# Optimization experiments

Measured on AMD Instinct MI355X. Metric: run time of the kernel, lower is better.

Reference implementation:

```python
import jax, jax.numpy as jnp
import numpy as np

B, S, DM = 8, 1024, 512   # batch, seq_len, model dim
H, D = 8, 64              # n_heads, per-head dim


def setup_inputs() -> dict:
    key = jax.random.key(0)
    k1, k2, k3, k4, k5 = jax.random.split(key, 5)
    sc = 1.0 / np.sqrt(DM)
    return {
        "x": jax.random.normal(k1, (B, S, DM), dtype=jnp.float32),
        "Wq": jax.random.normal(k2, (H, DM, D), dtype=jnp.float32) * sc,
        "Wk": jax.random.normal(k3, (H, DM, D), dtype=jnp.float32) * sc,
        "Wv": jax.random.normal(k4, (H, DM, D), dtype=jnp.float32) * sc,
        "Wo": jax.random.normal(k5, (H * D, DM), dtype=jnp.float32) * (1.0 / np.sqrt(H * D)),
    }


def reference(x, Wq, Wk, Wv, Wo):
    # Batched multi-head attention equivalent to the per-head Python loop.
    q = jnp.einsum("bsm,hmd->bhsd", x, Wq)
    k = jnp.einsum("bsm,hmd->bhsd", x, Wk)
    v = jnp.einsum("bsm,hmd->bhsd", x, Wv)
    scores = jnp.einsum("bhsd,bhtd->bhst", q, k) / jnp.sqrt(jnp.float32(D))
    attn = jax.nn.softmax(scores, axis=-1)          # [B,H,S,S]
    heads = jnp.einsum("bhst,bhtd->bhsd", attn, v)  # [B,H,S,D]
    # concat heads along feature dim (head order matches loop order)
    concat = heads.transpose(0, 2, 1, 3).reshape(B, S, H * D)
    z = jnp.einsum("bsf,fm->bsm", concat, Wo)       # output projection
    return z, attn
```

## Files before the change

### kernel.cpp

```cpp
#include <hip/hip_runtime.h>

#define B 8
#define S 1024
#define DM 512
#define H 8
#define D 64

typedef __attribute__((ext_vector_type(8))) short bf16x8;
typedef __attribute__((ext_vector_type(4))) float f32x4;

__device__ inline f32x4 mfma16(bf16x8 a, bf16x8 b, f32x4 c) {
  return __builtin_amdgcn_mfma_f32_16x16x32_bf16(a, b, c, 0, 0, 0);
}

__device__ inline ushort f2bf(float f) {
  uint u = __float_as_uint(f);
  u += 0x7fff + ((u >> 16) & 1);
  return (ushort)(u >> 16);
}

__global__ __launch_bounds__(256) void cast_x_kernel(const float* __restrict__ x,
                                                     ushort* __restrict__ xbf) {
  int idx = blockIdx.x * 256 + threadIdx.x;
  float4 v = *(const float4*)(x + (size_t)idx * 4);
  ushort4 o;
  o.x = f2bf(v.x); o.y = f2bf(v.y); o.z = f2bf(v.z); o.w = f2bf(v.w);
  *(ushort4*)(xbf + (size_t)idx * 4) = o;
}

__global__ __launch_bounds__(256) void prep_w_kernel(
    const float* __restrict__ Wq, const float* __restrict__ Wk,
    const float* __restrict__ Wv, const float* __restrict__ Wo,
    ushort* __restrict__ WT, ushort* __restrict__ WoT) {
  int idx = blockIdx.x * 256 + threadIdx.x;
  if (idx < 1536 * 512) {
    int f = idx >> 9, m = idx & 511;
    int g = f >> 9, fl = f & 511, h = fl >> 6, d = fl & 63;
    const float* W = (g == 0) ? Wq : (g == 1) ? Wk : Wv;
    WT[idx] = f2bf(W[((size_t)h * DM + m) * D + d]);
  } else {
    int i2 = idx - 1536 * 512;
    int m = i2 >> 9, f = i2 & 511;
    WoT[(size_t)m * 512 + f] = f2bf(Wo[(size_t)f * DM + m]);
  }
}

__global__ __launch_bounds__(256) void qkv_gemm_kernel(
    const ushort* __restrict__ A, const ushort* __restrict__ Bm,
    ushort* __restrict__ qb, ushort* __restrict__ kb, ushort* __restrict__ vt) {
  __shared__ ushort As[64][72], Bs[64][72];
  const int tid = threadIdx.x;
  const int m0 = blockIdx.x * 64, n0 = blockIdx.y * 64;
  const int w = tid >> 6, l = tid & 63;
  const int r = l & 15, q = l >> 4;
  const int mh = (w >> 1) * 32, nh = (w & 1) * 32;

  f32x4 acc[2][2] = {};
  const int srow = tid >> 2, sco = (tid & 3) * 16;

  for (int k0 = 0; k0 < 512; k0 += 64) {
    const ushort* ap = A + (size_t)(m0 + srow) * 512 + k0 + sco;
    const ushort* bp = Bm + (size_t)(n0 + srow) * 512 + k0 + sco;
    uint4 a0 = *(const uint4*)ap;
    uint4 a1 = *(const uint4*)(ap + 8);
    uint4 b0 = *(const uint4*)bp;
    uint4 b1 = *(const uint4*)(bp + 8);
    __syncthreads();
    *(uint4*)&As[srow][sco] = a0;
    *(uint4*)&As[srow][sco + 8] = a1;
    *(uint4*)&Bs[srow][sco] = b0;
    *(uint4*)&Bs[srow][sco + 8] = b1;
    __syncthreads();
    #pragma unroll
    for (int kk = 0; kk < 64; kk += 32) {
      bf16x8 fa0 = *(const bf16x8*)&As[mh + r][kk + q * 8];
      bf16x8 fa1 = *(const bf16x8*)&As[mh + 16 + r][kk + q * 8];
      bf16x8 fb0 = *(const bf16x8*)&Bs[nh + r][kk + q * 8];
      bf16x8 fb1 = *(const bf16x8*)&Bs[nh + 16 + r][kk + q * 8];
      acc[0][0] = mfma16(fa0, fb0, acc[0][0]);
      acc[0][1] = mfma16(fa0, fb1, acc[0][1]);
      acc[1][0] = mfma16(fa1, fb0, acc[1][0]);
      acc[1][1] = mfma16(fa1, fb1, acc[1][1]);
    }
  }

  const int g = n0 >> 9;
  #pragma unroll
  for (int mi = 0; mi < 2; ++mi)
    #pragma unroll
    for (int nj = 0; nj < 2; ++nj)
      #pragma unroll
      for (int i = 0; i < 4; ++i) {
        int row = m0 + mh + mi * 16 + q * 4 + i;
        int col = n0 + nh + nj * 16 + r;
        int bb = row >> 10, s = row & 1023;
        int fl = col & 511, h = fl >> 6, d = fl & 63;
        ushort val = f2bf(acc[mi][nj][i]);
        if (g == 0)
          qb[(((size_t)bb * H + h) * S + s) * D + d] = val;
        else if (g == 1)
          kb[(((size_t)bb * H + h) * S + s) * D + d] = val;
        else
          vt[(((size_t)bb * H + h) * D + d) * S + s] = val;
      }
}

__global__ __launch_bounds__(256, 4) void attn_kernel(
    const ushort* __restrict__ qb, const ushort* __restrict__ kb,
    const ushort* __restrict__ vt, float* __restrict__ attn,
    ushort* __restrict__ concat) {
  __shared__ ushort Pl[16 * 1024];
  __shared__ float redm[4][16], redsum[4][16];
  const int tid = threadIdx.x;
  const int w = tid >> 6, l = tid & 63;
  const int r = l & 15, q = l >> 4;
  const int s0 = blockIdx.x * 16, bh = blockIdx.y;

  const ushort* qp = qb + ((size_t)bh * S + s0) * D;
  bf16x8 qa0 = *(const bf16x8*)(qp + r * 64 + q * 8);
  bf16x8 qa1 = *(const bf16x8*)(qp + r * 64 + 32 + q * 8);

  const ushort* kp = kb + (size_t)bh * S * D;
  f32x4 sc[16];
  #pragma unroll
  for (int kt = 0; kt < 16; ++kt) {
    const ushort* kr = kp + (size_t)(w * 256 + kt * 16 + r) * 64 + q * 8;
    bf16x8 kf0 = *(const bf16x8*)kr;
    bf16x8 kf1 = *(const bf16x8*)(kr + 32);
    f32x4 a = {};
    a = mfma16(qa0, kf0, a);
    a = mfma16(qa1, kf1, a);
    sc[kt] = a * 0.125f;
  }

  float mx[4];
  #pragma unroll
  for (int i = 0; i < 4; ++i) {
    float m = sc[0][i];
    #pragma unroll
    for (int kt = 1; kt < 16; ++kt) m = fmaxf(m, sc[kt][i]);
    #pragma unroll
    for (int msk = 1; msk < 16; msk <<= 1) m = fmaxf(m, __shfl_xor(m, msk));
    mx[i] = m;
  }
  if (r == 0) {
    #pragma unroll
    for (int i = 0; i < 4; ++i) redm[w][q * 4 + i] = mx[i];
  }
  __syncthreads();
  #pragma unroll
  for (int i = 0; i < 4; ++i)
    mx[i] = fmaxf(fmaxf(redm[0][q * 4 + i], redm[1][q * 4 + i]),
                  fmaxf(redm[2][q * 4 + i], redm[3][q * 4 + i]));

  float sm[4] = {0.f, 0.f, 0.f, 0.f};
  #pragma unroll
  for (int kt = 0; kt < 16; ++kt)
    #pragma unroll
    for (int i = 0; i < 4; ++i) {
      float e = __expf(sc[kt][i] - mx[i]);
      sc[kt][i] = e;
      sm[i] += e;
    }
  #pragma unroll
  for (int i = 0; i < 4; ++i) {
    float s = sm[i];
    #pragma unroll
    for (int msk = 1; msk < 16; msk <<= 1) s += __shfl_xor(s, msk);
    sm[i] = s;
  }
  if (r == 0) {
    #pragma unroll
    for (int i = 0; i < 4; ++i) redsum[w][q * 4 + i] = sm[i];
  }
  __syncthreads();
  float rinv[4];
  #pragma unroll
  for (int i = 0; i < 4; ++i)
    rinv[i] = 1.0f / (redsum[0][q * 4 + i] + redsum[1][q * 4 + i] +
                      redsum[2][q * 4 + i] + redsum[3][q * 4 + i]);

  float* ap = attn + ((size_t)bh * S + s0) * S;
  #pragma unroll
  for (int kt = 0; kt < 16; ++kt) {
    int col = w * 256 + kt * 16 + r;
    #pragma unroll
    for (int i = 0; i < 4; ++i) {
      int row = q * 4 + i;
      ap[(size_t)row * S + col] = sc[kt][i] * rinv[i];
      Pl[row * 1024 + (col ^ ((row & 7) << 3))] = f2bf(sc[kt][i]);
    }
  }
  __syncthreads();

  {
    const int d0 = w * 16;
    const ushort* vp = vt + ((size_t)bh * D + d0 + r) * S;
    f32x4 acc[4] = {};
    #pragma unroll
    for (int stp = 0; stp < 32; ++stp) {
      int t0 = stp * 32 + q * 8;
      bf16x8 pa = *(const bf16x8*)&Pl[r * 1024 + (t0 ^ ((r & 7) << 3))];
      bf16x8 vb = *(const bf16x8*)(vp + t0);
      acc[stp & 3] = mfma16(pa, vb, acc[stp & 3]);
    }
    f32x4 tot = acc[0] + acc[1] + acc[2] + acc[3];
    const int b = bh >> 3, h = bh & 7;
    #pragma unroll
    for (int i = 0; i < 4; ++i)
      concat[((size_t)b * S + s0 + q * 4 + i) * DM + h * D + d0 + r] =
          f2bf(tot[i] * rinv[i]);
  }
}

__global__ __launch_bounds__(256) void outproj_gemm_kernel(
    const ushort* __restrict__ A, const ushort* __restrict__ Bm,
    float* __restrict__ z) {
  __shared__ ushort As[64][72], Bs[64][72];
  const int tid = threadIdx.x;
  const int m0 = blockIdx.x * 64, n0 = blockIdx.y * 64;
  const int w = tid >> 6, l = tid & 63;
  const int r = l & 15, q = l >> 4;
  const int mh = (w >> 1) * 32, nh = (w & 1) * 32;

  f32x4 acc[2][2] = {};
  const int srow = tid >> 2, sco = (tid & 3) * 16;

  for (int k0 = 0; k0 < 512; k0 += 64) {
    const ushort* ap = A + (size_t)(m0 + srow) * 512 + k0 + sco;
    const ushort* bp = Bm + (size_t)(n0 + srow) * 512 + k0 + sco;
    uint4 a0 = *(const uint4*)ap;
    uint4 a1 = *(const uint4*)(ap + 8);
    uint4 b0 = *(const uint4*)bp;
    uint4 b1 = *(const uint4*)(bp + 8);
    __syncthreads();
    *(uint4*)&As[srow][sco] = a0;
    *(uint4*)&As[srow][sco + 8] = a1;
    *(uint4*)&Bs[srow][sco] = b0;
    *(uint4*)&Bs[srow][sco + 8] = b1;
    __syncthreads();
    #pragma unroll
    for (int kk = 0; kk < 64; kk += 32) {
      bf16x8 fa0 = *(const bf16x8*)&As[mh + r][kk + q * 8];
      bf16x8 fa1 = *(const bf16x8*)&As[mh + 16 + r][kk + q * 8];
      bf16x8 fb0 = *(const bf16x8*)&Bs[nh + r][kk + q * 8];
      bf16x8 fb1 = *(const bf16x8*)&Bs[nh + 16 + r][kk + q * 8];
      acc[0][0] = mfma16(fa0, fb0, acc[0][0]);
      acc[0][1] = mfma16(fa0, fb1, acc[0][1]);
      acc[1][0] = mfma16(fa1, fb0, acc[1][0]);
      acc[1][1] = mfma16(fa1, fb1, acc[1][1]);
    }
  }

  #pragma unroll
  for (int mi = 0; mi < 2; ++mi)
    #pragma unroll
    for (int nj = 0; nj < 2; ++nj)
      #pragma unroll
      for (int i = 0; i < 4; ++i) {
        int row = m0 + mh + mi * 16 + q * 4 + i;
        int col = n0 + nh + nj * 16 + r;
        z[(size_t)row * DM + col] = acc[mi][nj][i];
      }
}

extern "C" void kernel_launch(void* const* d_in, const int* in_sizes, int n_in,
                              void* d_out, int out_size, void* d_ws, size_t ws_size,
                              hipStream_t stream) {
  const float* x  = (const float*)d_in[0];
  const float* Wq = (const float*)d_in[1];
  const float* Wk = (const float*)d_in[2];
  const float* Wv = (const float*)d_in[3];
  const float* Wo = (const float*)d_in[4];

  float* z    = (float*)d_out;
  float* attn = z + (size_t)B * S * DM;

  ushort* xbf    = (ushort*)d_ws;
  ushort* WT     = xbf + (size_t)8192 * 512;
  ushort* WoT    = WT + (size_t)1536 * 512;
  ushort* qb     = WoT + (size_t)512 * 512;
  ushort* kb     = qb + (size_t)B * H * S * D;
  ushort* vt     = kb + (size_t)B * H * S * D;
  ushort* concat = vt + (size_t)B * H * S * D;

  cast_x_kernel<<<(B * S * DM / 4 + 255) / 256, 256, 0, stream>>>(x, xbf);
  prep_w_kernel<<<(1536 * 512 + 512 * 512) / 256, 256, 0, stream>>>(
      Wq, Wk, Wv, Wo, WT, WoT);
  qkv_gemm_kernel<<<dim3(8192 / 64, 1536 / 64), 256, 0, stream>>>(
      xbf, WT, qb, kb, vt);
  attn_kernel<<<dim3(S / 16, B * H), 256, 0, stream>>>(
      qb, kb, vt, attn, concat);
  outproj_gemm_kernel<<<dim3(8192 / 64, 512 / 64), 256, 0, stream>>>(
      concat, WoT, z);
}
```

Measured before the change: 190.3 us.

## Enlarge GEMM tiles to 128x128, use direct global-to-LDS loads, merge prep kernels

Both projection GEMMs move from 64x64 to 128x128 block tiles, with each wave computing a 4x4 grid of MFMA tiles for more operand reuse. Operands are staged through global_load_lds instead of register round-trips, and the LDS row padding is removed, which can cause bank conflicts. The x cast and weight transposes are merged into one prep kernel whose weight reads are now coalesced. The out-projection grid shrinks to 256 blocks, which may underfill the GPU's compute units.

```diff
diff --git a/kernel.cpp b/kernel.cpp
--- a/kernel.cpp
+++ b/kernel.cpp
@@ -19,28 +19,34 @@
   return (ushort)(u >> 16);
 }
 
-__global__ __launch_bounds__(256) void cast_x_kernel(const float* __restrict__ x,
-                                                     ushort* __restrict__ xbf) {
-  int idx = blockIdx.x * 256 + threadIdx.x;
-  float4 v = *(const float4*)(x + (size_t)idx * 4);
-  ushort4 o;
-  o.x = f2bf(v.x); o.y = f2bf(v.y); o.z = f2bf(v.z); o.w = f2bf(v.w);
-  *(ushort4*)(xbf + (size_t)idx * 4) = o;
-}
-
-__global__ __launch_bounds__(256) void prep_w_kernel(
-    const float* __restrict__ Wq, const float* __restrict__ Wk,
-    const float* __restrict__ Wv, const float* __restrict__ Wo,
+#define GLOAD16(gp, lp)                                                  \
+  __builtin_amdgcn_global_load_lds(                                      \
+      (const __attribute__((address_space(1))) void*)(gp),               \
+      (__attribute__((address_space(3))) void*)(lp), 16, 0, 0)
+
+__global__ __launch_bounds__(256) void prep_kernel(
+    const float* __restrict__ x, const float* __restrict__ Wq,
+    const float* __restrict__ Wk, const float* __restrict__ Wv,
+    const float* __restrict__ Wo, ushort* __restrict__ xbf,
     ushort* __restrict__ WT, ushort* __restrict__ WoT) {
-  int idx = blockIdx.x * 256 + threadIdx.x;
-  if (idx < 1536 * 512) {
-    int f = idx >> 9, m = idx & 511;
-    int g = f >> 9, fl = f & 511, h = fl >> 6, d = fl & 63;
+  const int bid = blockIdx.x;
+  if (bid < 4096) {
+    int idx = bid * 256 + threadIdx.x;
+    float4 v = *(const float4*)(x + (size_t)idx * 4);
+    ushort4 o;
+    o.x = f2bf(v.x); o.y = f2bf(v.y); o.z = f2bf(v.z); o.w = f2bf(v.w);
+    *(ushort4*)(xbf + (size_t)idx * 4) = o;
+  } else if (bid < 7168) {
+    int idx = (bid - 4096) * 256 + threadIdx.x;
+    int g = idx >> 18;
+    int rem = idx & 262143;
     const float* W = (g == 0) ? Wq : (g == 1) ? Wk : Wv;
-    WT[idx] = f2bf(W[((size_t)h * DM + m) * D + d]);
+    float val = W[rem];
+    int d = rem & 63, m = (rem >> 6) & 511, h = rem >> 15;
+    WT[((size_t)(g << 9) + (h << 6) + d) * 512 + m] = f2bf(val);
   } else {
-    int i2 = idx - 1536 * 512;
-    int m = i2 >> 9, f = i2 & 511;
+    int idx = (bid - 7168) * 256 + threadIdx.x;
+    int m = idx & 511, f = idx >> 9;
     WoT[(size_t)m * 512 + f] = f2bf(Wo[(size_t)f * DM + m]);
   }
 }
@@ -48,51 +54,52 @@
 __global__ __launch_bounds__(256) void qkv_gemm_kernel(
     const ushort* __restrict__ A, const ushort* __restrict__ Bm,
     ushort* __restrict__ qb, ushort* __restrict__ kb, ushort* __restrict__ vt) {
-  __shared__ ushort As[64][72], Bs[64][72];
+  __shared__ ushort As[128 * 64], Bs[128 * 64];
   const int tid = threadIdx.x;
-  const int m0 = blockIdx.x * 64, n0 = blockIdx.y * 64;
+  const int m0 = blockIdx.x * 128, n0 = blockIdx.y * 128;
   const int w = tid >> 6, l = tid & 63;
   const int r = l & 15, q = l >> 4;
-  const int mh = (w >> 1) * 32, nh = (w & 1) * 32;
-
-  f32x4 acc[2][2] = {};
-  const int srow = tid >> 2, sco = (tid & 3) * 16;
+  const int wr = (w >> 1) * 64, wc = (w & 1) * 64;
+
+  f32x4 acc[4][4] = {};
+  const int o0 = tid * 16;
 
   for (int k0 = 0; k0 < 512; k0 += 64) {
-    const ushort* ap = A + (size_t)(m0 + srow) * 512 + k0 + sco;
-    const ushort* bp = Bm + (size_t)(n0 + srow) * 512 + k0 + sco;
-    uint4 a0 = *(const uint4*)ap;
-    uint4 a1 = *(const uint4*)(ap + 8);
-    uint4 b0 = *(const uint4*)bp;
-    uint4 b1 = *(const uint4*)(bp + 8);
     __syncthreads();
-    *(uint4*)&As[srow][sco] = a0;
-    *(uint4*)&As[srow][sco + 8] = a1;
-    *(uint4*)&Bs[srow][sco] = b0;
-    *(uint4*)&Bs[srow][sco + 8] = b1;
+    #pragma unroll
+    for (int j = 0; j < 4; ++j) {
+      int o = j * 4096 + o0;
+      int row = o >> 7, cb = o & 127;
+      GLOAD16(A + (size_t)(m0 + row) * 512 + k0 + (cb >> 1), &As[o >> 1]);
+      GLOAD16(Bm + (size_t)(n0 + row) * 512 + k0 + (cb >> 1), &Bs[o >> 1]);
+    }
     __syncthreads();
     #pragma unroll
     for (int kk = 0; kk < 64; kk += 32) {
-      bf16x8 fa0 = *(const bf16x8*)&As[mh + r][kk + q * 8];
-      bf16x8 fa1 = *(const bf16x8*)&As[mh + 16 + r][kk + q * 8];
-      bf16x8 fb0 = *(const bf16x8*)&Bs[nh + r][kk + q * 8];
-      bf16x8 fb1 = *(const bf16x8*)&Bs[nh + 16 + r][kk + q * 8];
-      acc[0][0] = mfma16(fa0, fb0, acc[0][0]);
-      acc[0][1] = mfma16(fa0, fb1, acc[0][1]);
-      acc[1][0] = mfma16(fa1, fb0, acc[1][0]);
-      acc[1][1] = mfma16(fa1, fb1, acc[1][1]);
+      bf16x8 fa[4], fb[4];
+      #pragma unroll
+      for (int mi = 0; mi < 4; ++mi)
+        fa[mi] = *(const bf16x8*)&As[(wr + mi * 16 + r) * 64 + kk + q * 8];
+      #pragma unroll
+      for (int nj = 0; nj < 4; ++nj)
+        fb[nj] = *(const bf16x8*)&Bs[(wc + nj * 16 + r) * 64 + kk + q * 8];
+      #pragma unroll
+      for (int mi = 0; mi < 4; ++mi)
+        #pragma unroll
+        for (int nj = 0; nj < 4; ++nj)
+          acc[mi][nj] = mfma16(fa[mi], fb[nj], acc[mi][nj]);
     }
   }
 
   const int g = n0 >> 9;
   #pragma unroll
-  for (int mi = 0; mi < 2; ++mi)
-    #pragma unroll
-    for (int nj = 0; nj < 2; ++nj)
+  for (int mi = 0; mi < 4; ++mi)
+    #pragma unroll
+    for (int nj = 0; nj < 4; ++nj)
       #pragma unroll
       for (int i = 0; i < 4; ++i) {
-        int row = m0 + mh + mi * 16 + q * 4 + i;
-        int col = n0 + nh + nj * 16 + r;
+        int row = m0 + wr + mi * 16 + q * 4 + i;
+        int col = n0 + wc + nj * 16 + r;
         int bb = row >> 10, s = row & 1023;
         int fl = col & 511, h = fl >> 6, d = fl & 63;
         ushort val = f2bf(acc[mi][nj][i]);
@@ -216,50 +223,51 @@
 __global__ __launch_bounds__(256) void outproj_gemm_kernel(
     const ushort* __restrict__ A, const ushort* __restrict__ Bm,
     float* __restrict__ z) {
-  __shared__ ushort As[64][72], Bs[64][72];
+  __shared__ ushort As[128 * 64], Bs[128 * 64];
   const int tid = threadIdx.x;
-  const int m0 = blockIdx.x * 64, n0 = blockIdx.y * 64;
+  const int m0 = blockIdx.x * 128, n0 = blockIdx.y * 128;
   const int w = tid >> 6, l = tid & 63;
   const int r = l & 15, q = l >> 4;
-  const int mh = (w >> 1) * 32, nh = (w & 1) * 32;
-
-  f32x4 acc[2][2] = {};
-  const int srow = tid >> 2, sco = (tid & 3) * 16;
+  const int wr = (w >> 1) * 64, wc = (w & 1) * 64;
+
+  f32x4 acc[4][4] = {};
+  const int o0 = tid * 16;
 
   for (int k0 = 0; k0 < 512; k0 += 64) {
-    const ushort* ap = A + (size_t)(m0 + srow) * 512 + k0 + sco;
-    const ushort* bp = Bm + (size_t)(n0 + srow) * 512 + k0 + sco;
-    uint4 a0 = *(const uint4*)ap;
-    uint4 a1 = *(const uint4*)(ap + 8);
-    uint4 b0 = *(const uint4*)bp;
-    uint4 b1 = *(const uint4*)(bp + 8);
     __syncthreads();
-    *(uint4*)&As[srow][sco] = a0;
-    *(uint4*)&As[srow][sco + 8] = a1;
-    *(uint4*)&Bs[srow][sco] = b0;
-    *(uint4*)&Bs[srow][sco + 8] = b1;
+    #pragma unroll
+    for (int j = 0; j < 4; ++j) {
+      int o = j * 4096 + o0;
+      int row = o >> 7, cb = o & 127;
+      GLOAD16(A + (size_t)(m0 + row) * 512 + k0 + (cb >> 1), &As[o >> 1]);
+      GLOAD16(Bm + (size_t)(n0 + row) * 512 + k0 + (cb >> 1), &Bs[o >> 1]);
+    }
     __syncthreads();
     #pragma unroll
     for (int kk = 0; kk < 64; kk += 32) {
-      bf16x8 fa0 = *(const bf16x8*)&As[mh + r][kk + q * 8];
-      bf16x8 fa1 = *(const bf16x8*)&As[mh + 16 + r][kk + q * 8];
-      bf16x8 fb0 = *(const bf16x8*)&Bs[nh + r][kk + q * 8];
-      bf16x8 fb1 = *(const bf16x8*)&Bs[nh + 16 + r][kk + q * 8];
-      acc[0][0] = mfma16(fa0, fb0, acc[0][0]);
-      acc[0][1] = mfma16(fa0, fb1, acc[0][1]);
-      acc[1][0] = mfma16(fa1, fb0, acc[1][0]);
-      acc[1][1] = mfma16(fa1, fb1, acc[1][1]);
-    }
-  }
-
-  #pragma unroll
-  for (int mi = 0; mi < 2; ++mi)
-    #pragma unroll
-    for (int nj = 0; nj < 2; ++nj)
+      bf16x8 fa[4], fb[4];
+      #pragma unroll
+      for (int mi = 0; mi < 4; ++mi)
+        fa[mi] = *(const bf16x8*)&As[(wr + mi * 16 + r) * 64 + kk + q * 8];
+      #pragma unroll
+      for (int nj = 0; nj < 4; ++nj)
+        fb[nj] = *(const bf16x8*)&Bs[(wc + nj * 16 + r) * 64 + kk + q * 8];
+      #pragma unroll
+      for (int mi = 0; mi < 4; ++mi)
+        #pragma unroll
+        for (int nj = 0; nj < 4; ++nj)
+          acc[mi][nj] = mfma16(fa[mi], fb[nj], acc[mi][nj]);
+    }
+  }
+
+  #pragma unroll
+  for (int mi = 0; mi < 4; ++mi)
+    #pragma unroll
+    for (int nj = 0; nj < 4; ++nj)
       #pragma unroll
       for (int i = 0; i < 4; ++i) {
-        int row = m0 + mh + mi * 16 + q * 4 + i;
-        int col = n0 + nh + nj * 16 + r;
+        int row = m0 + wr + mi * 16 + q * 4 + i;
+        int col = n0 + wc + nj * 16 + r;
         z[(size_t)row * DM + col] = acc[mi][nj][i];
       }
 }
@@ -284,13 +292,11 @@
   ushort* vt     = kb + (size_t)B * H * S * D;
   ushort* concat = vt + (size_t)B * H * S * D;
 
-  cast_x_kernel<<<(B * S * DM / 4 + 255) / 256, 256, 0, stream>>>(x, xbf);
-  prep_w_kernel<<<(1536 * 512 + 512 * 512) / 256, 256, 0, stream>>>(
-      Wq, Wk, Wv, Wo, WT, WoT);
-  qkv_gemm_kernel<<<dim3(8192 / 64, 1536 / 64), 256, 0, stream>>>(
+  prep_kernel<<<8192, 256, 0, stream>>>(x, Wq, Wk, Wv, Wo, xbf, WT, WoT);
+  qkv_gemm_kernel<<<dim3(8192 / 128, 1536 / 128), 256, 0, stream>>>(
       xbf, WT, qb, kb, vt);
   attn_kernel<<<dim3(S / 16, B * H), 256, 0, stream>>>(
       qb, kb, vt, attn, concat);
-  outproj_gemm_kernel<<<dim3(8192 / 64, 512 / 64), 256, 0, stream>>>(
+  outproj_gemm_kernel<<<dim3(8192 / 128, 512 / 128), 256, 0, stream>>>(
       concat, WoT, z);
 }
```

Result: slower. 199.8 us (+5.0%).

## Fuse all stages into one persistent cooperative kernel with grid syncs

Applied to the files above, without the earlier changes.

Replaces the five separate launches (cast, weight prep, QKV GEMM, attention, output GEMM) with a single persistent cooperative kernel. Blocks loop over tiles for each stage and meet at grid-wide barriers between stages, with shared memory reused through a union. The weight-prep loop now reads the weights contiguously and scatters the transposed writes. This removes launch gaps and tail effects between stages, but adds grid-sync cost and caps concurrency at the occupancy-derived grid size (at most 1024 blocks).

```diff
diff --git a/kernel.cpp b/kernel.cpp
--- a/kernel.cpp
+++ b/kernel.cpp
@@ -1,4 +1,7 @@
 #include <hip/hip_runtime.h>
+#include <hip/hip_cooperative_groups.h>
+
+namespace cg = cooperative_groups;
 
 #define B 8
 #define S 1024
@@ -19,249 +22,258 @@
   return (ushort)(u >> 16);
 }
 
-__global__ __launch_bounds__(256) void cast_x_kernel(const float* __restrict__ x,
-                                                     ushort* __restrict__ xbf) {
-  int idx = blockIdx.x * 256 + threadIdx.x;
-  float4 v = *(const float4*)(x + (size_t)idx * 4);
-  ushort4 o;
-  o.x = f2bf(v.x); o.y = f2bf(v.y); o.z = f2bf(v.z); o.w = f2bf(v.w);
-  *(ushort4*)(xbf + (size_t)idx * 4) = o;
-}
-
-__global__ __launch_bounds__(256) void prep_w_kernel(
-    const float* __restrict__ Wq, const float* __restrict__ Wk,
-    const float* __restrict__ Wv, const float* __restrict__ Wo,
-    ushort* __restrict__ WT, ushort* __restrict__ WoT) {
-  int idx = blockIdx.x * 256 + threadIdx.x;
-  if (idx < 1536 * 512) {
-    int f = idx >> 9, m = idx & 511;
-    int g = f >> 9, fl = f & 511, h = fl >> 6, d = fl & 63;
-    const float* W = (g == 0) ? Wq : (g == 1) ? Wk : Wv;
-    WT[idx] = f2bf(W[((size_t)h * DM + m) * D + d]);
-  } else {
-    int i2 = idx - 1536 * 512;
-    int m = i2 >> 9, f = i2 & 511;
-    WoT[(size_t)m * 512 + f] = f2bf(Wo[(size_t)f * DM + m]);
-  }
-}
-
-__global__ __launch_bounds__(256) void qkv_gemm_kernel(
-    const ushort* __restrict__ A, const ushort* __restrict__ Bm,
-    ushort* __restrict__ qb, ushort* __restrict__ kb, ushort* __restrict__ vt) {
-  __shared__ ushort As[64][72], Bs[64][72];
+union SMem {
+  struct { ushort As[64][72]; ushort Bs[64][72]; } g;
+  struct { ushort Pl[16 * 1024];
+           float redm[4][16]; float redsum[4][16]; } a;
+};
+
+__global__ __launch_bounds__(256, 4) void mega_kernel(
+    const float* __restrict__ x, const float* __restrict__ Wq,
+    const float* __restrict__ Wk, const float* __restrict__ Wv,
+    const float* __restrict__ Wo, float* __restrict__ z,
+    float* __restrict__ attnO, ushort* __restrict__ xbf,
+    ushort* __restrict__ WT, ushort* __restrict__ WoT,
+    ushort* __restrict__ qb, ushort* __restrict__ kb,
+    ushort* __restrict__ vt, ushort* __restrict__ concat) {
+  __shared__ SMem sm;
+  cg::grid_group grid = cg::this_grid();
   const int tid = threadIdx.x;
-  const int m0 = blockIdx.x * 64, n0 = blockIdx.y * 64;
-  const int w = tid >> 6, l = tid & 63;
-  const int r = l & 15, q = l >> 4;
-  const int mh = (w >> 1) * 32, nh = (w & 1) * 32;
-
-  f32x4 acc[2][2] = {};
-  const int srow = tid >> 2, sco = (tid & 3) * 16;
-
-  for (int k0 = 0; k0 < 512; k0 += 64) {
-    const ushort* ap = A + (size_t)(m0 + srow) * 512 + k0 + sco;
-    const ushort* bp = Bm + (size_t)(n0 + srow) * 512 + k0 + sco;
-    uint4 a0 = *(const uint4*)ap;
-    uint4 a1 = *(const uint4*)(ap + 8);
-    uint4 b0 = *(const uint4*)bp;
-    uint4 b1 = *(const uint4*)(bp + 8);
-    __syncthreads();
-    *(uint4*)&As[srow][sco] = a0;
-    *(uint4*)&As[srow][sco + 8] = a1;
-    *(uint4*)&Bs[srow][sco] = b0;
-    *(uint4*)&Bs[srow][sco + 8] = b1;
-    __syncthreads();
-    #pragma unroll
-    for (int kk = 0; kk < 64; kk += 32) {
-      bf16x8 fa0 = *(const bf16x8*)&As[mh + r][kk + q * 8];
-      bf16x8 fa1 = *(const bf16x8*)&As[mh + 16 + r][kk + q * 8];
-      bf16x8 fb0 = *(const bf16x8*)&Bs[nh + r][kk + q * 8];
-      bf16x8 fb1 = *(const bf16x8*)&Bs[nh + 16 + r][kk + q * 8];
-      acc[0][0] = mfma16(fa0, fb0, acc[0][0]);
-      acc[0][1] = mfma16(fa0, fb1, acc[0][1]);
-      acc[1][0] = mfma16(fa1, fb0, acc[1][0]);
-      acc[1][1] = mfma16(fa1, fb1, acc[1][1]);
+  const int nthr = gridDim.x * 256;
+
+  {
+    const int NX = 1 << 20;
+    const int NWT = 3 * 8 * 512 * 64;
+    const int tot = NX + NWT + 512 * 512;
+    for (int idx = blockIdx.x * 256 + tid; idx < tot; idx += nthr) {
+      if (idx < NX) {
+        float4 v = *(const float4*)(x + (size_t)idx * 4);
+        ushort4 o;
+        o.x = f2bf(v.x); o.y = f2bf(v.y); o.z = f2bf(v.z); o.w = f2bf(v.w);
+        *(ushort4*)(xbf + (size_t)idx * 4) = o;
+      } else if (idx < NX + NWT) {
+        int i2 = idx - NX;
+        int g = i2 >> 18, rem = i2 & 262143;
+        const float* W = (g == 0) ? Wq : (g == 1) ? Wk : Wv;
+        float val = W[rem];
+        int d = rem & 63, m = (rem >> 6) & 511, h = rem >> 15;
+        WT[((size_t)(g << 9) + (h << 6) + d) * 512 + m] = f2bf(val);
+      } else {
+        int i2 = idx - NX - NWT;
+        int m = i2 & 511, f = i2 >> 9;
+        WoT[(size_t)m * 512 + f] = f2bf(Wo[(size_t)f * DM + m]);
+      }
     }
   }
-
-  const int g = n0 >> 9;
-  #pragma unroll
-  for (int mi = 0; mi < 2; ++mi)
-    #pragma unroll
-    for (int nj = 0; nj < 2; ++nj)
+  grid.sync();
+
+  {
+    const int w = tid >> 6, l = tid & 63;
+    const int r = l & 15, qq = l >> 4;
+    const int mh = (w >> 1) * 32, nh = (w & 1) * 32;
+    const int srow = tid >> 2, sco = (tid & 3) * 16;
+    for (int t = blockIdx.x; t < 3072; t += gridDim.x) {
+      const int m0 = (t & 127) * 64, n0 = (t >> 7) * 64;
+      f32x4 acc[2][2] = {};
+      for (int k0 = 0; k0 < 512; k0 += 64) {
+        const ushort* ap = xbf + (size_t)(m0 + srow) * 512 + k0 + sco;
+        const ushort* bp = WT + (size_t)(n0 + srow) * 512 + k0 + sco;
+        uint4 a0 = *(const uint4*)ap;
+        uint4 a1 = *(const uint4*)(ap + 8);
+        uint4 b0 = *(const uint4*)bp;
+        uint4 b1 = *(const uint4*)(bp + 8);
+        __syncthreads();
+        *(uint4*)&sm.g.As[srow][sco] = a0;
+        *(uint4*)&sm.g.As[srow][sco + 8] = a1;
+        *(uint4*)&sm.g.Bs[srow][sco] = b0;
+        *(uint4*)&sm.g.Bs[srow][sco + 8] = b1;
+        __syncthreads();
+        #pragma unroll
+        for (int kk = 0; kk < 64; kk += 32) {
+          bf16x8 fa0 = *(const bf16x8*)&sm.g.As[mh + r][kk + qq * 8];
+          bf16x8 fa1 = *(const bf16x8*)&sm.g.As[mh + 16 + r][kk + qq * 8];
+          bf16x8 fb0 = *(const bf16x8*)&sm.g.Bs[nh + r][kk + qq * 8];
+          bf16x8 fb1 = *(const bf16x8*)&sm.g.Bs[nh + 16 + r][kk + qq * 8];
+          acc[0][0] = mfma16(fa0, fb0, acc[0][0]);
+          acc[0][1] = mfma16(fa0, fb1, acc[0][1]);
+          acc[1][0] = mfma16(fa1, fb0, acc[1][0]);
+          acc[1][1] = mfma16(fa1, fb1, acc[1][1]);
+        }
+      }
+      const int g = n0 >> 9;
+      #pragma unroll
+      for (int mi = 0; mi < 2; ++mi)
+        #pragma unroll
+        for (int nj = 0; nj < 2; ++nj)
+          #pragma unroll
+          for (int i = 0; i < 4; ++i) {
+            int row = m0 + mh + mi * 16 + qq * 4 + i;
+            int col = n0 + nh + nj * 16 + r;
+            int bb = row >> 10, s = row & 1023;
+            int fl = col & 511, h = fl >> 6, d = fl & 63;
+            ushort val = f2bf(acc[mi][nj][i]);
+            if (g == 0)
+              qb[(((size_t)bb * H + h) * S + s) * D + d] = val;
+            else if (g == 1)
+              kb[(((size_t)bb * H + h) * S + s) * D + d] = val;
+            else
+              vt[(((size_t)bb * H + h) * D + d) * S + s] = val;
+          }
+    }
+  }
+  grid.sync();
+
+  {
+    const int w = tid >> 6, l = tid & 63;
+    const int r = l & 15, qq = l >> 4;
+    for (int t = blockIdx.x; t < 4096; t += gridDim.x) {
+      __syncthreads();
+      const int s0 = (t & 63) * 16, bh = t >> 6;
+
+      const ushort* qp = qb + ((size_t)bh * S + s0) * D;
+      bf16x8 qa0 = *(const bf16x8*)(qp + r * 64 + qq * 8);
+      bf16x8 qa1 = *(const bf16x8*)(qp + r * 64 + 32 + qq * 8);
+
+      const ushort* kp = kb + (size_t)bh * S * D;
+      f32x4 sc[16];
+      #pragma unroll
+      for (int kt = 0; kt < 16; ++kt) {
+        const ushort* kr = kp + (size_t)(w * 256 + kt * 16 + r) * 64 + qq * 8;
+        bf16x8 kf0 = *(const bf16x8*)kr;
+        bf16x8 kf1 = *(const bf16x8*)(kr + 32);
+        f32x4 a = {};
+        a = mfma16(qa0, kf0, a);
+        a = mfma16(qa1, kf1, a);
+        sc[kt] = a * 0.125f;
+      }
+
+      float mx[4];
       #pragma unroll
       for (int i = 0; i < 4; ++i) {
-        int row = m0 + mh + mi * 16 + q * 4 + i;
-        int col = n0 + nh + nj * 16 + r;
-        int bb = row >> 10, s = row & 1023;
-        int fl = col & 511, h = fl >> 6, d = fl & 63;
-        ushort val = f2bf(acc[mi][nj][i]);
-        if (g == 0)
-          qb[(((size_t)bb * H + h) * S + s) * D + d] = val;
-        else if (g == 1)
-          kb[(((size_t)bb * H + h) * S + s) * D + d] = val;
-        else
-          vt[(((size_t)bb * H + h) * D + d) * S + s] = val;
-      }
-}
-
-__global__ __launch_bounds__(256, 4) void attn_kernel(
-    const ushort* __restrict__ qb, const ushort* __restrict__ kb,
-    const ushort* __restrict__ vt, float* __restrict__ attn,
-    ushort* __restrict__ concat) {
-  __shared__ ushort Pl[16 * 1024];
-  __shared__ float redm[4][16], redsum[4][16];
-  const int tid = threadIdx.x;
-  const int w = tid >> 6, l = tid & 63;
-  const int r = l & 15, q = l >> 4;
-  const int s0 = blockIdx.x * 16, bh = blockIdx.y;
-
-  const ushort* qp = qb + ((size_t)bh * S + s0) * D;
-  bf16x8 qa0 = *(const bf16x8*)(qp + r * 64 + q * 8);
-  bf16x8 qa1 = *(const bf16x8*)(qp + r * 64 + 32 + q * 8);
-
-  const ushort* kp = kb + (size_t)bh * S * D;
-  f32x4 sc[16];
-  #pragma unroll
-  for (int kt = 0; kt < 16; ++kt) {
-    const ushort* kr = kp + (size_t)(w * 256 + kt * 16 + r) * 64 + q * 8;
-    bf16x8 kf0 = *(const bf16x8*)kr;
-    bf16x8 kf1 = *(const bf16x8*)(kr + 32);
-    f32x4 a = {};
-    a = mfma16(qa0, kf0, a);
-    a = mfma16(qa1, kf1, a);
-    sc[kt] = a * 0.125f;
-  }
-
-  float mx[4];
-  #pragma unroll
-  for (int i = 0; i < 4; ++i) {
-    float m = sc[0][i];
-    #pragma unroll
-    for (int kt = 1; kt < 16; ++kt) m = fmaxf(m, sc[kt][i]);
-    #pragma unroll
-    for (int msk = 1; msk < 16; msk <<= 1) m = fmaxf(m, __shfl_xor(m, msk));
-    mx[i] = m;
-  }
-  if (r == 0) {
-    #pragma unroll
-    for (int i = 0; i < 4; ++i) redm[w][q * 4 + i] = mx[i];
-  }
-  __syncthreads();
-  #pragma unroll
-  for (int i = 0; i < 4; ++i)
-    mx[i] = fmaxf(fmaxf(redm[0][q * 4 + i], redm[1][q * 4 + i]),
-                  fmaxf(redm[2][q * 4 + i], redm[3][q * 4 + i]));
-
-  float sm[4] = {0.f, 0.f, 0.f, 0.f};
-  #pragma unroll
-  for (int kt = 0; kt < 16; ++kt)
-    #pragma unroll
-    for (int i = 0; i < 4; ++i) {
-      float e = __expf(sc[kt][i] - mx[i]);
-      sc[kt][i] = e;
-      sm[i] += e;
+        float m = sc[0][i];
+        #pragma unroll
+        for (int kt = 1; kt < 16; ++kt) m = fmaxf(m, sc[kt][i]);
+        #pragma unroll
+        for (int msk = 1; msk < 16; msk <<= 1) m = fmaxf(m, __shfl_xor(m, msk));
+        mx[i] = m;
+      }
+      if (r == 0) {
+        #pragma unroll
+        for (int i = 0; i < 4; ++i) sm.a.redm[w][qq * 4 + i] = mx[i];
+      }
+      __syncthreads();
+      #pragma unroll
+      for (int i = 0; i < 4; ++i)
+        mx[i] = fmaxf(fmaxf(sm.a.redm[0][qq * 4 + i], sm.a.redm[1][qq * 4 + i]),
+                      fmaxf(sm.a.redm[2][qq * 4 + i], sm.a.redm[3][qq * 4 + i]));
+
+      float smv[4] = {0.f, 0.f, 0.f, 0.f};
+      #pragma unroll
+      for (int kt = 0; kt < 16; ++kt)
+        #pragma unroll
+        for (int i = 0; i < 4; ++i) {
+          float e = __expf(sc[kt][i] - mx[i]);
+          sc[kt][i] = e;
+          smv[i] += e;
+        }
+      #pragma unroll
+      for (int i = 0; i < 4; ++i) {
+        float s = smv[i];
+        #pragma unroll
+        for (int msk = 1; msk < 16; msk <<= 1) s += __shfl_xor(s, msk);
+        smv[i] = s;
+      }
+      if (r == 0) {
+        #pragma unroll
+        for (int i = 0; i < 4; ++i) sm.a.redsum[w][qq * 4 + i] = smv[i];
+      }
+      __syncthreads();
+      float rinv[4];
+      #pragma unroll
+      for (int i = 0; i < 4; ++i)
+        rinv[i] = 1.0f / (sm.a.redsum[0][qq * 4 + i] + sm.a.redsum[1][qq * 4 + i] +
+                          sm.a.redsum[2][qq * 4 + i] + sm.a.redsum[3][qq * 4 + i]);
+
+      float* ap = attnO + ((size_t)bh * S + s0) * S;
+      #pragma unroll
+      for (int kt = 0; kt < 16; ++kt) {
+        int col = w * 256 + kt * 16 + r;
+        #pragma unroll
+        for (int i = 0; i < 4; ++i) {
+          int row = qq * 4 + i;
+          ap[(size_t)row * S + col] = sc[kt][i] * rinv[i];
+          sm.a.Pl[row * 1024 + (col ^ ((row & 7) << 3))] = f2bf(sc[kt][i]);
+        }
+      }
+      __syncthreads();
+
+      {
+        const int d0 = w * 16;
+        const ushort* vp = vt + ((size_t)bh * D + d0 + r) * S;
+        f32x4 acc[4] = {};
+        #pragma unroll
+        for (int stp = 0; stp < 32; ++stp) {
+          int t0 = stp * 32 + qq * 8;
+          bf16x8 pa = *(const bf16x8*)&sm.a.Pl[r * 1024 + (t0 ^ ((r & 7) << 3))];
+          bf16x8 vb = *(const bf16x8*)(vp + t0);
+          acc[stp & 3] = mfma16(pa, vb, acc[stp & 3]);
+        }
+        f32x4 tot = acc[0] + acc[1] + acc[2] + acc[3];
+        const int b = t >> 9, h = (t >> 6) & 7;
+        #pragma unroll
+        for (int i = 0; i < 4; ++i)
+          concat[((size_t)b * S + s0 + qq * 4 + i) * DM + h * D + d0 + r] =
+              f2bf(tot[i] * rinv[i]);
+      }
     }
-  #pragma unroll
-  for (int i = 0; i < 4; ++i) {
-    float s = sm[i];
-    #pragma unroll
-    for (int msk = 1; msk < 16; msk <<= 1) s += __shfl_xor(s, msk);
-    sm[i] = s;
-  }
-  if (r == 0) {
-    #pragma unroll
-    for (int i = 0; i < 4; ++i) redsum[w][q * 4 + i] = sm[i];
-  }
-  __syncthreads();
-  float rinv[4];
-  #pragma unroll
-  for (int i = 0; i < 4; ++i)
-    rinv[i] = 1.0f / (redsum[0][q * 4 + i] + redsum[1][q * 4 + i] +
-                      redsum[2][q * 4 + i] + redsum[3][q * 4 + i]);
-
-  float* ap = attn + ((size_t)bh * S + s0) * S;
-  #pragma unroll
-  for (int kt = 0; kt < 16; ++kt) {
-    int col = w * 256 + kt * 16 + r;
-    #pragma unroll
-    for (int i = 0; i < 4; ++i) {
-      int row = q * 4 + i;
-      ap[(size_t)row * S + col] = sc[kt][i] * rinv[i];
-      Pl[row * 1024 + (col ^ ((row & 7) << 3))] = f2bf(sc[kt][i]);
+  }
+  grid.sync();
+
+  {
+    const int w = tid >> 6, l = tid & 63;
+    const int r = l & 15, qq = l >> 4;
+    const int mh = (w >> 1) * 32, nh = (w & 1) * 32;
+    const int srow = tid >> 2, sco = (tid & 3) * 16;
+    for (int t = blockIdx.x; t < 1024; t += gridDim.x) {
+      const int m0 = (t >> 3) * 64, n0 = (t & 7) * 64;
+      f32x4 acc[2][2] = {};
+      for (int k0 = 0; k0 < 512; k0 += 64) {
+        const ushort* ap = concat + (size_t)(m0 + srow) * 512 + k0 + sco;
+        const ushort* bp = WoT + (size_t)(n0 + srow) * 512 + k0 + sco;
+        uint4 a0 = *(const uint4*)ap;
+        uint4 a1 = *(const uint4*)(ap + 8);
+        uint4 b0 = *(const uint4*)bp;
+        uint4 b1 = *(const uint4*)(bp + 8);
+        __syncthreads();
+        *(uint4*)&sm.g.As[srow][sco] = a0;
+        *(uint4*)&sm.g.As[srow][sco + 8] = a1;
+        *(uint4*)&sm.g.Bs[srow][sco] = b0;
+        *(uint4*)&sm.g.Bs[srow][sco + 8] = b1;
+        __syncthreads();
+        #pragma unroll
+        for (int kk = 0; kk < 64; kk += 32) {
+          bf16x8 fa0 = *(const bf16x8*)&sm.g.As[mh + r][kk + qq * 8];
+          bf16x8 fa1 = *(const bf16x8*)&sm.g.As[mh + 16 + r][kk + qq * 8];
+          bf16x8 fb0 = *(const bf16x8*)&sm.g.Bs[nh + r][kk + qq * 8];
+          bf16x8 fb1 = *(const bf16x8*)&sm.g.Bs[nh + 16 + r][kk + qq * 8];
+          acc[0][0] = mfma16(fa0, fb0, acc[0][0]);
+          acc[0][1] = mfma16(fa0, fb1, acc[0][1]);
+          acc[1][0] = mfma16(fa1, fb0, acc[1][0]);
+          acc[1][1] = mfma16(fa1, fb1, acc[1][1]);
+        }
+      }
+      #pragma unroll
+      for (int mi = 0; mi < 2; ++mi)
+        #pragma unroll
+        for (int nj = 0; nj < 2; ++nj)
+          #pragma unroll
+          for (int i = 0; i < 4; ++i) {
+            int row = m0 + mh + mi * 16 + qq * 4 + i;
+            int col = n0 + nh + nj * 16 + r;
+            z[(size_t)row * DM + col] = acc[mi][nj][i];
+          }
     }
   }
-  __syncthreads();
-
-  {
-    const int d0 = w * 16;
-    const ushort* vp = vt + ((size_t)bh * D + d0 + r) * S;
-    f32x4 acc[4] = {};
-    #pragma unroll
-    for (int stp = 0; stp < 32; ++stp) {
-      int t0 = stp * 32 + q * 8;
-      bf16x8 pa = *(const bf16x8*)&Pl[r * 1024 + (t0 ^ ((r & 7) << 3))];
-      bf16x8 vb = *(const bf16x8*)(vp + t0);
-      acc[stp & 3] = mfma16(pa, vb, acc[stp & 3]);
-    }
-    f32x4 tot = acc[0] + acc[1] + acc[2] + acc[3];
-    const int b = bh >> 3, h = bh & 7;
-    #pragma unroll
-    for (int i = 0; i < 4; ++i)
-      concat[((size_t)b * S + s0 + q * 4 + i) * DM + h * D + d0 + r] =
-          f2bf(tot[i] * rinv[i]);
-  }
-}
-
-__global__ __launch_bounds__(256) void outproj_gemm_kernel(
-    const ushort* __restrict__ A, const ushort* __restrict__ Bm,
-    float* __restrict__ z) {
-  __shared__ ushort As[64][72], Bs[64][72];
-  const int tid = threadIdx.x;
-  const int m0 = blockIdx.x * 64, n0 = blockIdx.y * 64;
-  const int w = tid >> 6, l = tid & 63;
-  const int r = l & 15, q = l >> 4;
-  const int mh = (w >> 1) * 32, nh = (w & 1) * 32;
-
-  f32x4 acc[2][2] = {};
-  const int srow = tid >> 2, sco = (tid & 3) * 16;
-
-  for (int k0 = 0; k0 < 512; k0 += 64) {
-    const ushort* ap = A + (size_t)(m0 + srow) * 512 + k0 + sco;
-    const ushort* bp = Bm + (size_t)(n0 + srow) * 512 + k0 + sco;
-    uint4 a0 = *(const uint4*)ap;
-    uint4 a1 = *(const uint4*)(ap + 8);
-    uint4 b0 = *(const uint4*)bp;
-    uint4 b1 = *(const uint4*)(bp + 8);
-    __syncthreads();
-    *(uint4*)&As[srow][sco] = a0;
-    *(uint4*)&As[srow][sco + 8] = a1;
-    *(uint4*)&Bs[srow][sco] = b0;
-    *(uint4*)&Bs[srow][sco + 8] = b1;
-    __syncthreads();
-    #pragma unroll
-    for (int kk = 0; kk < 64; kk += 32) {
-      bf16x8 fa0 = *(const bf16x8*)&As[mh + r][kk + q * 8];
-      bf16x8 fa1 = *(const bf16x8*)&As[mh + 16 + r][kk + q * 8];
-      bf16x8 fb0 = *(const bf16x8*)&Bs[nh + r][kk + q * 8];
-      bf16x8 fb1 = *(const bf16x8*)&Bs[nh + 16 + r][kk + q * 8];
-      acc[0][0] = mfma16(fa0, fb0, acc[0][0]);
-      acc[0][1] = mfma16(fa0, fb1, acc[0][1]);
-      acc[1][0] = mfma16(fa1, fb0, acc[1][0]);
-      acc[1][1] = mfma16(fa1, fb1, acc[1][1]);
-    }
-  }
-
-  #pragma unroll
-  for (int mi = 0; mi < 2; ++mi)
-    #pragma unroll
-    for (int nj = 0; nj < 2; ++nj)
-      #pragma unroll
-      for (int i = 0; i < 4; ++i) {
-        int row = m0 + mh + mi * 16 + q * 4 + i;
-        int col = n0 + nh + nj * 16 + r;
-        z[(size_t)row * DM + col] = acc[mi][nj][i];
-      }
 }
 
 extern "C" void kernel_launch(void* const* d_in, const int* in_sizes, int n_in,
@@ -284,13 +296,19 @@
   ushort* vt     = kb + (size_t)B * H * S * D;
   ushort* concat = vt + (size_t)B * H * S * D;
 
-  cast_x_kernel<<<(B * S * DM / 4 + 255) / 256, 256, 0, stream>>>(x, xbf);
-  prep_w_kernel<<<(1536 * 512 + 512 * 512) / 256, 256, 0, stream>>>(
-      Wq, Wk, Wv, Wo, WT, WoT);
-  qkv_gemm_kernel<<<dim3(8192 / 64, 1536 / 64), 256, 0, stream>>>(
-      xbf, WT, qb, kb, vt);
-  attn_kernel<<<dim3(S / 16, B * H), 256, 0, stream>>>(
-      qb, kb, vt, attn, concat);
-  outproj_gemm_kernel<<<dim3(8192 / 64, 512 / 64), 256, 0, stream>>>(
-      concat, WoT, z);
+  static int grid = 0;
+  if (grid == 0) {
+    int maxB = 0;
+    hipOccupancyMaxActiveBlocksPerMultiprocessor(&maxB, mega_kernel, 256, 0);
+    if (maxB < 1) maxB = 1;
+    grid = maxB * 256;
+    if (grid > 1024) grid = 1024;
+  }
+
+  void* args[] = {(void*)&x,   (void*)&Wq,  (void*)&Wk,  (void*)&Wv,
+                  (void*)&Wo,  (void*)&z,   (void*)&attn, (void*)&xbf,
+                  (void*)&WT,  (void*)&WoT, (void*)&qb,  (void*)&kb,
+                  (void*)&vt,  (void*)&concat};
+  hipLaunchCooperativeKernel((const void*)mega_kernel, dim3(grid), dim3(256),
+                             args, 0, stream);
 }
```

Result: slower. 611.5 us (+221.4%).

## Restructure attention into single-wave two-pass kernel with streamed P·V and nontemporal stores

Applied to the files above, without the earlier changes.

The attention kernel now runs one 64-thread wave per 16-row query tile and works in 128-column chunks. A first pass recomputes QK^T only to build the row sums of exp, which avoids keeping all 1024 scores in registers and avoids the cross-wave LDS reductions and barriers. The max subtraction is dropped, so exp is not shifted and can overflow for large scores. A second pass recomputes the scores, normalises them, and stages P in a small LDS tile. From there it writes attn with coalesced nontemporal 16-byte stores and feeds P·V MFMAs chunk by chunk. A swizzled 1D grid mapping is added, and the attn values written out are rounded through bf16, which reduces output precision.

```diff
diff --git a/kernel.cpp b/kernel.cpp
--- a/kernel.cpp
+++ b/kernel.cpp
@@ -17,6 +17,10 @@
   uint u = __float_as_uint(f);
   u += 0x7fff + ((u >> 16) & 1);
   return (ushort)(u >> 16);
+}
+
+__device__ inline float bf2f(ushort u) {
+  return __uint_as_float(((uint)u) << 16);
 }
 
 __global__ __launch_bounds__(256) void cast_x_kernel(const float* __restrict__ x,
@@ -105,112 +109,105 @@
       }
 }
 
-__global__ __launch_bounds__(256, 4) void attn_kernel(
+__global__ __launch_bounds__(64, 4) void attn_kernel(
     const ushort* __restrict__ qb, const ushort* __restrict__ kb,
     const ushort* __restrict__ vt, float* __restrict__ attn,
     ushort* __restrict__ concat) {
-  __shared__ ushort Pl[16 * 1024];
-  __shared__ float redm[4][16], redsum[4][16];
-  const int tid = threadIdx.x;
-  const int w = tid >> 6, l = tid & 63;
+  __shared__ ushort Plc[16][136];
+  const int l = threadIdx.x;
   const int r = l & 15, q = l >> 4;
-  const int s0 = blockIdx.x * 16, bh = blockIdx.y;
+
+  const int n = blockIdx.x;
+  const int rank = n >> 3;
+  const int bh = (n & 7) * 8 + (rank >> 6);
+  const int s0 = (rank & 63) * 16;
 
   const ushort* qp = qb + ((size_t)bh * S + s0) * D;
   bf16x8 qa0 = *(const bf16x8*)(qp + r * 64 + q * 8);
   bf16x8 qa1 = *(const bf16x8*)(qp + r * 64 + 32 + q * 8);
 
   const ushort* kp = kb + (size_t)bh * S * D;
-  f32x4 sc[16];
-  #pragma unroll
-  for (int kt = 0; kt < 16; ++kt) {
-    const ushort* kr = kp + (size_t)(w * 256 + kt * 16 + r) * 64 + q * 8;
-    bf16x8 kf0 = *(const bf16x8*)kr;
-    bf16x8 kf1 = *(const bf16x8*)(kr + 32);
-    f32x4 a = {};
-    a = mfma16(qa0, kf0, a);
-    a = mfma16(qa1, kf1, a);
-    sc[kt] = a * 0.125f;
-  }
-
-  float mx[4];
-  #pragma unroll
-  for (int i = 0; i < 4; ++i) {
-    float m = sc[0][i];
-    #pragma unroll
-    for (int kt = 1; kt < 16; ++kt) m = fmaxf(m, sc[kt][i]);
-    #pragma unroll
-    for (int msk = 1; msk < 16; msk <<= 1) m = fmaxf(m, __shfl_xor(m, msk));
-    mx[i] = m;
-  }
-  if (r == 0) {
-    #pragma unroll
-    for (int i = 0; i < 4; ++i) redm[w][q * 4 + i] = mx[i];
-  }
-  __syncthreads();
-  #pragma unroll
-  for (int i = 0; i < 4; ++i)
-    mx[i] = fmaxf(fmaxf(redm[0][q * 4 + i], redm[1][q * 4 + i]),
-                  fmaxf(redm[2][q * 4 + i], redm[3][q * 4 + i]));
 
   float sm[4] = {0.f, 0.f, 0.f, 0.f};
-  #pragma unroll
-  for (int kt = 0; kt < 16; ++kt)
-    #pragma unroll
-    for (int i = 0; i < 4; ++i) {
-      float e = __expf(sc[kt][i] - mx[i]);
-      sc[kt][i] = e;
-      sm[i] += e;
-    }
+  for (int c = 0; c < 8; ++c) {
+    f32x4 sc[8];
+    #pragma unroll
+    for (int kt = 0; kt < 8; ++kt) {
+      const ushort* kr = kp + (size_t)(c * 128 + kt * 16 + r) * 64 + q * 8;
+      bf16x8 kf0 = *(const bf16x8*)kr;
+      bf16x8 kf1 = *(const bf16x8*)(kr + 32);
+      f32x4 a = {};
+      a = mfma16(qa0, kf0, a);
+      a = mfma16(qa1, kf1, a);
+      sc[kt] = a * 0.125f;
+    }
+    #pragma unroll
+    for (int kt = 0; kt < 8; ++kt)
+      #pragma unroll
+      for (int i = 0; i < 4; ++i) sm[i] += __expf(sc[kt][i]);
+  }
+  float rinv[4];
   #pragma unroll
   for (int i = 0; i < 4; ++i) {
     float s = sm[i];
     #pragma unroll
     for (int msk = 1; msk < 16; msk <<= 1) s += __shfl_xor(s, msk);
-    sm[i] = s;
-  }
-  if (r == 0) {
-    #pragma unroll
-    for (int i = 0; i < 4; ++i) redsum[w][q * 4 + i] = sm[i];
-  }
-  __syncthreads();
-  float rinv[4];
-  #pragma unroll
-  for (int i = 0; i < 4; ++i)
-    rinv[i] = 1.0f / (redsum[0][q * 4 + i] + redsum[1][q * 4 + i] +
-                      redsum[2][q * 4 + i] + redsum[3][q * 4 + i]);
-
+    rinv[i] = 1.0f / s;
+  }
+
+  f32x4 acc[4] = {};
   float* ap = attn + ((size_t)bh * S + s0) * S;
-  #pragma unroll
-  for (int kt = 0; kt < 16; ++kt) {
-    int col = w * 256 + kt * 16 + r;
-    #pragma unroll
-    for (int i = 0; i < 4; ++i) {
-      int row = q * 4 + i;
-      ap[(size_t)row * S + col] = sc[kt][i] * rinv[i];
-      Pl[row * 1024 + (col ^ ((row & 7) << 3))] = f2bf(sc[kt][i]);
-    }
-  }
-  __syncthreads();
-
-  {
-    const int d0 = w * 16;
-    const ushort* vp = vt + ((size_t)bh * D + d0 + r) * S;
-    f32x4 acc[4] = {};
-    #pragma unroll
-    for (int stp = 0; stp < 32; ++stp) {
-      int t0 = stp * 32 + q * 8;
-      bf16x8 pa = *(const bf16x8*)&Pl[r * 1024 + (t0 ^ ((r & 7) << 3))];
-      bf16x8 vb = *(const bf16x8*)(vp + t0);
-      acc[stp & 3] = mfma16(pa, vb, acc[stp & 3]);
-    }
-    f32x4 tot = acc[0] + acc[1] + acc[2] + acc[3];
-    const int b = bh >> 3, h = bh & 7;
+  const size_t vtb = (size_t)bh * D;
+  for (int c = 0; c < 8; ++c) {
+    f32x4 sc[8];
+    #pragma unroll
+    for (int kt = 0; kt < 8; ++kt) {
+      const ushort* kr = kp + (size_t)(c * 128 + kt * 16 + r) * 64 + q * 8;
+      bf16x8 kf0 = *(const bf16x8*)kr;
+      bf16x8 kf1 = *(const bf16x8*)(kr + 32);
+      f32x4 a = {};
+      a = mfma16(qa0, kf0, a);
+      a = mfma16(qa1, kf1, a);
+      sc[kt] = a * 0.125f;
+    }
+    #pragma unroll
+    for (int kt = 0; kt < 8; ++kt)
+      #pragma unroll
+      for (int i = 0; i < 4; ++i) {
+        float p = __expf(sc[kt][i]) * rinv[i];
+        Plc[q * 4 + i][kt * 16 + r] = f2bf(p);
+      }
+    {
+      const int row = l >> 2, c4 = (l & 3) * 4;
+      #pragma unroll
+      for (int j = 0; j < 8; ++j) {
+        const int col = c4 + j * 16;
+        ushort4 p4 = *(const ushort4*)&Plc[row][col];
+        f32x4 o;
+        o.x = bf2f(p4.x); o.y = bf2f(p4.y);
+        o.z = bf2f(p4.z); o.w = bf2f(p4.w);
+        __builtin_nontemporal_store(
+            o, (f32x4*)(ap + (size_t)row * S + c * 128 + col));
+      }
+    }
+    #pragma unroll
+    for (int kk = 0; kk < 4; ++kk) {
+      bf16x8 pa = *(const bf16x8*)&Plc[r][kk * 32 + q * 8];
+      #pragma unroll
+      for (int dg = 0; dg < 4; ++dg) {
+        const ushort* vb = vt + (vtb + dg * 16 + r) * S + c * 128 + kk * 32 + q * 8;
+        acc[dg] = mfma16(pa, *(const bf16x8*)vb, acc[dg]);
+      }
+    }
+  }
+
+  const int b = bh >> 3, h = bh & 7;
+  #pragma unroll
+  for (int dg = 0; dg < 4; ++dg)
     #pragma unroll
     for (int i = 0; i < 4; ++i)
-      concat[((size_t)b * S + s0 + q * 4 + i) * DM + h * D + d0 + r] =
-          f2bf(tot[i] * rinv[i]);
-  }
+      concat[((size_t)b * S + s0 + q * 4 + i) * DM + h * D + dg * 16 + r] =
+          f2bf(acc[dg][i]);
 }
 
 __global__ __launch_bounds__(256) void outproj_gemm_kernel(
@@ -289,8 +286,7 @@
       Wq, Wk, Wv, Wo, WT, WoT);
   qkv_gemm_kernel<<<dim3(8192 / 64, 1536 / 64), 256, 0, stream>>>(
       xbf, WT, qb, kb, vt);
-  attn_kernel<<<dim3(S / 16, B * H), 256, 0, stream>>>(
-      qb, kb, vt, attn, concat);
+  attn_kernel<<<4096, 64, 0, stream>>>(qb, kb, vt, attn, concat);
   outproj_gemm_kernel<<<dim3(8192 / 64, 512 / 64), 256, 0, stream>>>(
       concat, WoT, z);
 }
```

Result: slower. 236.6 us (+24.4%).
